# Kernel tuning notes

Measured on AMD Instinct MI355X. Metric: run time of the kernel, lower is better.

Reference implementation:

```python
import jax, jax.numpy as jnp
import numpy as np

N_EDGES, N_CH = 4, 2
N_NODES = 8192
IN_C, OUT_C = 64, 64


def setup_inputs() -> dict:
    key = jax.random.key(0)
    k1, k2, k3, k4, k5 = jax.random.split(key, 5)
    A = jax.random.uniform(k1, (N_EDGES, N_NODES, N_NODES), dtype=jnp.float32)
    X = jax.random.normal(k2, (N_NODES, IN_C), dtype=jnp.float32)
    weight = jax.random.normal(k3, (N_EDGES, N_CH), dtype=jnp.float32)
    # torch Linear: weight [out, in], bias [out]
    lin_w = jax.random.normal(k4, (OUT_C, IN_C), dtype=jnp.float32) / np.sqrt(IN_C)
    lin_b = jax.random.normal(k5, (OUT_C,), dtype=jnp.float32) * 0.01
    bias = jnp.zeros((OUT_C,), dtype=jnp.float32)
    return {"A": A, "X": X, "weight": weight, "lin_w": lin_w, "lin_b": lin_b, "bias": bias}


def reference(A, X, weight, lin_w, lin_b, bias):
    # softmax over edge dim (dim=0), then the double loop collapses to a
    # per-edge scale: A_agg = sum_i (sum_j fw[i,j]) * A[i]
    fw = jax.nn.softmax(weight, axis=0)          # [E, C]
    scale = fw.sum(axis=1)                        # [E]
    A_agg = jnp.einsum('e,enm->nm', scale, A)     # [N, N]
    H = A_agg @ X                                 # [N, in_c]
    H = H @ lin_w.T + lin_b + bias                # [N, out_c]
    return H
```

## Files before the change

kernel.cpp:

```cpp
#include <hip/hip_runtime.h>
#include <math.h>


#define NN 8192
#define CH 64
#define RB 16
#define KT 128
#define NT (NN / KT)
#define NBLK (NN / RB)

#define A_BUF_F (4 * RB * KT)
#define OFF_AGG (2 * A_BUF_F)
#define AGG_STRIDE_S 136
#define AGG_F ((RB * AGG_STRIDE_S) / 2)
#define LDS_FLOATS (OFF_AGG + AGG_F)
#define HT_STRIDE 68
#define XFRAGS_PER_TILE 1024

typedef __attribute__((ext_vector_type(8))) short bf16x8;
typedef __attribute__((ext_vector_type(4))) float f32x4;

__device__ __forceinline__ void dma16(const float* g, float* l) {
  __builtin_amdgcn_global_load_lds(
      (const __attribute__((address_space(1))) void*)g,
      (__attribute__((address_space(3))) void*)l, 16, 0, 0);
}

__device__ __forceinline__ unsigned f2bfu(float f) {
  unsigned u = __float_as_uint(f);
  return (u + 0x7FFFu + ((u >> 16) & 1u)) >> 16;
}

__global__ __launch_bounds__(256)
void gtn_packX(const float* __restrict__ X, unsigned* __restrict__ ws) {
  const int F = blockIdx.x * 256 + threadIdx.x;
  const int t = F >> 10, rem = F & 1023;
  const int wv = rem >> 8, kt = (rem >> 6) & 3, lane = rem & 63;
  const int fm = lane & 15, fg = lane >> 4;
  const int c = wv * 16 + fm;
  const int bk = t * KT + kt * 32 + fg * 8;
  uint4 o;
  o.x = f2bfu(X[(size_t)(bk + 0) * CH + c]) | (f2bfu(X[(size_t)(bk + 1) * CH + c]) << 16);
  o.y = f2bfu(X[(size_t)(bk + 2) * CH + c]) | (f2bfu(X[(size_t)(bk + 3) * CH + c]) << 16);
  o.z = f2bfu(X[(size_t)(bk + 4) * CH + c]) | (f2bfu(X[(size_t)(bk + 5) * CH + c]) << 16);
  o.w = f2bfu(X[(size_t)(bk + 6) * CH + c]) | (f2bfu(X[(size_t)(bk + 7) * CH + c]) << 16);
  *(uint4*)&ws[(size_t)F * 4] = o;
}

template<bool PACKED>
__global__ __launch_bounds__(256, 2)
void gtn_fused(const float* __restrict__ A, const float* __restrict__ X,
               const uint4* __restrict__ Xp,
               const float* __restrict__ Wt, const float* __restrict__ lw,
               const float* __restrict__ lb, const float* __restrict__ bias,
               float* __restrict__ out) {
  __shared__ __align__(16) float arena[LDS_FLOATS];

  const int tid = threadIdx.x;
  const int n0  = blockIdx.x * RB;

  float sc0, sc1, sc2, sc3;
  {
    float a0 = Wt[0], a1 = Wt[2], a2 = Wt[4], a3 = Wt[6];
    float b0 = Wt[1], b1 = Wt[3], b2 = Wt[5], b3 = Wt[7];
    float ma = fmaxf(fmaxf(a0, a1), fmaxf(a2, a3));
    float mb = fmaxf(fmaxf(b0, b1), fmaxf(b2, b3));
    float ea0 = expf(a0 - ma), ea1 = expf(a1 - ma), ea2 = expf(a2 - ma), ea3 = expf(a3 - ma);
    float eb0 = expf(b0 - mb), eb1 = expf(b1 - mb), eb2 = expf(b2 - mb), eb3 = expf(b3 - mb);
    float ra = 1.f / (ea0 + ea1 + ea2 + ea3);
    float rb = 1.f / (eb0 + eb1 + eb2 + eb3);
    sc0 = ea0 * ra + eb0 * rb;  sc1 = ea1 * ra + eb1 * rb;
    sc2 = ea2 * ra + eb2 * rb;  sc3 = ea3 * ra + eb3 * rb;
  }

  const float* gA[8];
#pragma unroll
  for (int i = 0; i < 8; ++i) {
    const int g = tid + i * 256;
    const int e = g >> 9, r = (g >> 5) & 15, kq = g & 31;
    gA[i] = A + ((size_t)e << 26) + (size_t)(n0 + r) * NN + kq * 4;
  }

  const int rg = tid >> 4, cg = tid & 15;
  const int lane = tid & 63, wv = tid >> 6;
  const int ch0 = wv * 16;
  const int fm = lane & 15, fg = lane >> 4;

  auto issueA = [&](int u, int bi) {
    const size_t koff = (size_t)u * KT;
    float* Ad = &arena[bi * A_BUF_F];
#pragma unroll
    for (int i = 0; i < 8; ++i) dma16(gA[i] + koff, Ad + (tid + i * 256) * 4);
  };

  uint4 xcur[4], xnxt[4];
  auto loadX = [&](int u, uint4* dst) {
    if constexpr (PACKED) {
      const uint4* xb = Xp + (size_t)u * XFRAGS_PER_TILE + wv * 256 + lane;
#pragma unroll
      for (int kt = 0; kt < 4; ++kt) dst[kt] = xb[kt * 64];
    } else {
#pragma unroll
      for (int kt = 0; kt < 4; ++kt) {
        const int bk = u * KT + kt * 32 + fg * 8;
        unsigned p[4];
#pragma unroll
        for (int pj = 0; pj < 4; ++pj)
          p[pj] = f2bfu(X[(size_t)(bk + 2 * pj) * CH + ch0 + fm]) |
                  (f2bfu(X[(size_t)(bk + 2 * pj + 1) * CH + ch0 + fm]) << 16);
        dst[kt] = make_uint4(p[0], p[1], p[2], p[3]);
      }
    }
  };

  auto combine = [&](int bi) {
    const float* Ab = &arena[bi * A_BUF_F];
    short* aggW = (short*)&arena[OFF_AGG];
#pragma unroll
    for (int h = 0; h < 2; ++h) {
      float gx = 0.f, gy = 0.f, gz = 0.f, gw = 0.f;
#pragma unroll
      for (int e = 0; e < 4; ++e) {
        const float s = (e == 0) ? sc0 : (e == 1) ? sc1 : (e == 2) ? sc2 : sc3;
        float4 v = *(const float4*)&Ab[(e * RB + rg) * KT + h * 64 + cg * 4];
        gx = fmaf(s, v.x, gx); gy = fmaf(s, v.y, gy);
        gz = fmaf(s, v.z, gz); gw = fmaf(s, v.w, gw);
      }
      unsigned u0 = f2bfu(gx) | (f2bfu(gy) << 16);
      unsigned u1 = f2bfu(gz) | (f2bfu(gw) << 16);
      *(uint2*)&aggW[rg * AGG_STRIDE_S + h * 64 + cg * 4] = make_uint2(u0, u1);
    }
  };

  f32x4 acc = {0.f, 0.f, 0.f, 0.f};
  auto domfma = [&](const uint4* xf) {
    const short* aggS = (const short*)&arena[OFF_AGG];
#pragma unroll
    for (int kt = 0; kt < 4; ++kt) {
      bf16x8 af = *(const bf16x8*)&aggS[fm * AGG_STRIDE_S + kt * 32 + fg * 8];
      union { uint4 q; bf16x8 v; } xu; xu.q = xf[kt];
      acc = __builtin_amdgcn_mfma_f32_16x16x32_bf16(af, xu.v, acc, 0, 0, 0);
    }
  };

  issueA(0, 0);
  loadX(0, xcur);
  issueA(1, 1);

  for (int t = 0; t < NT; ++t) {
    const int b = t & 1;
    if constexpr (PACKED) {
      if (t < 2)            asm volatile("s_waitcnt vmcnt(12)\n\ts_barrier" ::: "memory");
      else if (t < NT - 1)  asm volatile("s_waitcnt vmcnt(16)\n\ts_barrier" ::: "memory");
      else                  asm volatile("s_waitcnt vmcnt(8)\n\ts_barrier" ::: "memory");
    } else {
      asm volatile("s_waitcnt vmcnt(0)\n\ts_barrier" ::: "memory");
    }

    combine(b);
    asm volatile("s_waitcnt lgkmcnt(0)\n\ts_barrier" ::: "memory");

    if (t + 2 < NT) issueA(t + 2, b);
    if (t + 1 < NT) loadX(t + 1, xnxt);

    domfma(xcur);
#pragma unroll
    for (int kt = 0; kt < 4; ++kt) xcur[kt] = xnxt[kt];
  }

  __syncthreads();
  float* hT = arena;
#pragma unroll
  for (int r = 0; r < 4; ++r)
    hT[(fg * 4 + r) * HT_STRIDE + ch0 + fm] = acc[r];
  __syncthreads();

  const int c0 = cg * 4;
  float s0 = lb[c0 + 0] + bias[c0 + 0];
  float s1 = lb[c0 + 1] + bias[c0 + 1];
  float s2 = lb[c0 + 2] + bias[c0 + 2];
  float s3 = lb[c0 + 3] + bias[c0 + 3];
#pragma unroll
  for (int k4 = 0; k4 < CH / 4; ++k4) {
    float4 hv = *(const float4*)&hT[rg * HT_STRIDE + k4 * 4];
    float4 w0 = *(const float4*)&lw[(size_t)(c0 + 0) * CH + k4 * 4];
    float4 w1 = *(const float4*)&lw[(size_t)(c0 + 1) * CH + k4 * 4];
    float4 w2 = *(const float4*)&lw[(size_t)(c0 + 2) * CH + k4 * 4];
    float4 w3 = *(const float4*)&lw[(size_t)(c0 + 3) * CH + k4 * 4];
    s0 += hv.x * w0.x + hv.y * w0.y + hv.z * w0.z + hv.w * w0.w;
    s1 += hv.x * w1.x + hv.y * w1.y + hv.z * w1.z + hv.w * w1.w;
    s2 += hv.x * w2.x + hv.y * w2.y + hv.z * w2.z + hv.w * w2.w;
    s3 += hv.x * w3.x + hv.y * w3.y + hv.z * w3.z + hv.w * w3.w;
  }
  *(float4*)&out[(size_t)(n0 + rg) * CH + c0] = make_float4(s0, s1, s2, s3);
}

extern "C" void kernel_launch(void* const* d_in, const int* in_sizes, int n_in,
                              void* d_out, int out_size, void* d_ws, size_t ws_size,
                              hipStream_t stream) {
  const float* A    = (const float*)d_in[0];
  const float* X    = (const float*)d_in[1];
  const float* Wt   = (const float*)d_in[2];
  const float* lw   = (const float*)d_in[3];
  const float* lb   = (const float*)d_in[4];
  const float* bias = (const float*)d_in[5];
  float* out = (float*)d_out;

  const size_t packBytes = (size_t)NT * XFRAGS_PER_TILE * 16;
  if (ws_size >= packBytes) {
    gtn_packX<<<dim3(256), 256, 0, stream>>>(X, (unsigned*)d_ws);
    gtn_fused<true><<<dim3(NBLK), 256, 0, stream>>>(
        A, X, (const uint4*)d_ws, Wt, lw, lb, bias, out);
  } else {
    gtn_fused<false><<<dim3(NBLK), 256, 0, stream>>>(
        A, X, nullptr, Wt, lw, lb, bias, out);
  }
}
```

Before: 200.9 us.

## Replace LDS DMA staging of A with register double-buffered loads

```diff
diff --git a/kernel.cpp b/kernel.cpp
--- a/kernel.cpp
+++ b/kernel.cpp
@@ -9,22 +9,13 @@
 #define NT (NN / KT)
 #define NBLK (NN / RB)
 
-#define A_BUF_F (4 * RB * KT)
-#define OFF_AGG (2 * A_BUF_F)
 #define AGG_STRIDE_S 136
-#define AGG_F ((RB * AGG_STRIDE_S) / 2)
-#define LDS_FLOATS (OFF_AGG + AGG_F)
+#define AGG_HALF (RB * AGG_STRIDE_S)
 #define HT_STRIDE 68
 #define XFRAGS_PER_TILE 1024
 
 typedef __attribute__((ext_vector_type(8))) short bf16x8;
 typedef __attribute__((ext_vector_type(4))) float f32x4;
-
-__device__ __forceinline__ void dma16(const float* g, float* l) {
-  __builtin_amdgcn_global_load_lds(
-      (const __attribute__((address_space(1))) void*)g,
-      (__attribute__((address_space(3))) void*)l, 16, 0, 0);
-}
 
 __device__ __forceinline__ unsigned f2bfu(float f) {
   unsigned u = __float_as_uint(f);
@@ -48,13 +39,14 @@
 }
 
 template<bool PACKED>
-__global__ __launch_bounds__(256, 2)
+__global__ __launch_bounds__(256, 3)
 void gtn_fused(const float* __restrict__ A, const float* __restrict__ X,
                const uint4* __restrict__ Xp,
                const float* __restrict__ Wt, const float* __restrict__ lw,
                const float* __restrict__ lb, const float* __restrict__ bias,
                float* __restrict__ out) {
-  __shared__ __align__(16) float arena[LDS_FLOATS];
+  __shared__ __align__(16) short aggS[2][AGG_HALF];
+  __shared__ __align__(16) float hT[RB * HT_STRIDE];
 
   const int tid = threadIdx.x;
   const int n0  = blockIdx.x * RB;
@@ -73,36 +65,33 @@
     sc2 = ea2 * ra + eb2 * rb;  sc3 = ea3 * ra + eb3 * rb;
   }
 
-  const float* gA[8];
-#pragma unroll
-  for (int i = 0; i < 8; ++i) {
-    const int g = tid + i * 256;
-    const int e = g >> 9, r = (g >> 5) & 15, kq = g & 31;
-    gA[i] = A + ((size_t)e << 26) + (size_t)(n0 + r) * NN + kq * 4;
-  }
-
   const int rg = tid >> 4, cg = tid & 15;
   const int lane = tid & 63, wv = tid >> 6;
   const int ch0 = wv * 16;
   const int fm = lane & 15, fg = lane >> 4;
 
-  auto issueA = [&](int u, int bi) {
-    const size_t koff = (size_t)u * KT;
-    float* Ad = &arena[bi * A_BUF_F];
+  const unsigned rowOff = (unsigned)((n0 + rg) * NN + cg * 4);
+
+  auto loadA = [&](int t, float4* d) {
+    const unsigned tOff = rowOff + (unsigned)(t * KT);
 #pragma unroll
-    for (int i = 0; i < 8; ++i) dma16(gA[i] + koff, Ad + (tid + i * 256) * 4);
+    for (int e = 0; e < 4; ++e) {
+      const float* Ae = A + ((size_t)e << 26);
+#pragma unroll
+      for (int h = 0; h < 2; ++h)
+        d[e * 2 + h] = *(const float4*)(Ae + tOff + h * 64);
+    }
   };
 
-  uint4 xcur[4], xnxt[4];
-  auto loadX = [&](int u, uint4* dst) {
+  auto loadX = [&](int t, uint4* dst) {
     if constexpr (PACKED) {
-      const uint4* xb = Xp + (size_t)u * XFRAGS_PER_TILE + wv * 256 + lane;
+      const uint4* xb = Xp + (size_t)t * XFRAGS_PER_TILE + wv * 256 + lane;
 #pragma unroll
       for (int kt = 0; kt < 4; ++kt) dst[kt] = xb[kt * 64];
     } else {
 #pragma unroll
       for (int kt = 0; kt < 4; ++kt) {
-        const int bk = u * KT + kt * 32 + fg * 8;
+        const int bk = t * KT + kt * 32 + fg * 8;
         unsigned p[4];
 #pragma unroll
         for (int pj = 0; pj < 4; ++pj)
@@ -113,63 +102,47 @@
     }
   };
 
-  auto combine = [&](int bi) {
-    const float* Ab = &arena[bi * A_BUF_F];
-    short* aggW = (short*)&arena[OFF_AGG];
+  auto combine = [&](const float4* a, int b) {
 #pragma unroll
     for (int h = 0; h < 2; ++h) {
-      float gx = 0.f, gy = 0.f, gz = 0.f, gw = 0.f;
-#pragma unroll
-      for (int e = 0; e < 4; ++e) {
-        const float s = (e == 0) ? sc0 : (e == 1) ? sc1 : (e == 2) ? sc2 : sc3;
-        float4 v = *(const float4*)&Ab[(e * RB + rg) * KT + h * 64 + cg * 4];
-        gx = fmaf(s, v.x, gx); gy = fmaf(s, v.y, gy);
-        gz = fmaf(s, v.z, gz); gw = fmaf(s, v.w, gw);
-      }
+      float4 v0 = a[0 + h], v1 = a[2 + h], v2 = a[4 + h], v3 = a[6 + h];
+      float gx = fmaf(sc3, v3.x, fmaf(sc2, v2.x, fmaf(sc1, v1.x, sc0 * v0.x)));
+      float gy = fmaf(sc3, v3.y, fmaf(sc2, v2.y, fmaf(sc1, v1.y, sc0 * v0.y)));
+      float gz = fmaf(sc3, v3.z, fmaf(sc2, v2.z, fmaf(sc1, v1.z, sc0 * v0.z)));
+      float gw = fmaf(sc3, v3.w, fmaf(sc2, v2.w, fmaf(sc1, v1.w, sc0 * v0.w)));
       unsigned u0 = f2bfu(gx) | (f2bfu(gy) << 16);
       unsigned u1 = f2bfu(gz) | (f2bfu(gw) << 16);
-      *(uint2*)&aggW[rg * AGG_STRIDE_S + h * 64 + cg * 4] = make_uint2(u0, u1);
+      *(uint2*)&aggS[b][rg * AGG_STRIDE_S + h * 64 + cg * 4] = make_uint2(u0, u1);
     }
   };
 
   f32x4 acc = {0.f, 0.f, 0.f, 0.f};
-  auto domfma = [&](const uint4* xf) {
-    const short* aggS = (const short*)&arena[OFF_AGG];
+  auto domfma = [&](int b, const uint4* xf) {
 #pragma unroll
     for (int kt = 0; kt < 4; ++kt) {
-      bf16x8 af = *(const bf16x8*)&aggS[fm * AGG_STRIDE_S + kt * 32 + fg * 8];
+      bf16x8 af = *(const bf16x8*)&aggS[b][fm * AGG_STRIDE_S + kt * 32 + fg * 8];
       union { uint4 q; bf16x8 v; } xu; xu.q = xf[kt];
       acc = __builtin_amdgcn_mfma_f32_16x16x32_bf16(af, xu.v, acc, 0, 0, 0);
     }
   };
 
-  issueA(0, 0);
-  loadX(0, xcur);
-  issueA(1, 1);
+  float4 aA[8], aB[8];
+  uint4  xA[4], xB[4];
+  loadA(0, aA); loadX(0, xA);
 
-  for (int t = 0; t < NT; ++t) {
-    const int b = t & 1;
-    if constexpr (PACKED) {
-      if (t < 2)            asm volatile("s_waitcnt vmcnt(12)\n\ts_barrier" ::: "memory");
-      else if (t < NT - 1)  asm volatile("s_waitcnt vmcnt(16)\n\ts_barrier" ::: "memory");
-      else                  asm volatile("s_waitcnt vmcnt(8)\n\ts_barrier" ::: "memory");
-    } else {
-      asm volatile("s_waitcnt vmcnt(0)\n\ts_barrier" ::: "memory");
-    }
+  for (int t = 0; t < NT; t += 2) {
+    loadA(t + 1, aB); loadX(t + 1, xB);
+    combine(aA, 0);
+    asm volatile("s_waitcnt lgkmcnt(0)\n\ts_barrier" ::: "memory");
+    domfma(0, xA);
 
-    combine(b);
+    if (t + 2 < NT) { loadA(t + 2, aA); loadX(t + 2, xA); }
+    combine(aB, 1);
     asm volatile("s_waitcnt lgkmcnt(0)\n\ts_barrier" ::: "memory");
-
-    if (t + 2 < NT) issueA(t + 2, b);
-    if (t + 1 < NT) loadX(t + 1, xnxt);
-
-    domfma(xcur);
-#pragma unroll
-    for (int kt = 0; kt < 4; ++kt) xcur[kt] = xnxt[kt];
+    domfma(1, xB);
   }
 
   __syncthreads();
-  float* hT = arena;
 #pragma unroll
   for (int r = 0; r < 4; ++r)
     hT[(fg * 4 + r) * HT_STRIDE + ch0 + fm] = acc[r];
```

Result: faster. 192.8 us (-4.1%).
